# Performance work log

Measured on AMD Instinct MI355X. Metric: run time of the kernel, lower is better.

Reference implementation:

```python
import jax, jax.numpy as jnp
import numpy as np

B, N, PREV, PRED, H = 16, 64, 6, 30, 256
E = N * (N - 1)
BN_EPS = 1e-5


def _mlp(x, W1, b1, W2, b2, gamma, beta):
    # Two-layer ELU MLP with batch norm over flattened (batch*rows) dim.
    h = jax.nn.elu(x @ W1 + b1)
    h = jax.nn.elu(h @ W2 + b2)
    b, n, d = h.shape
    f = h.reshape(b * n, d)
    mu = f.mean(axis=0)
    var = f.var(axis=0)
    f = (f - mu) * jax.lax.rsqrt(var + BN_EPS) * gamma + beta
    return f.reshape(b, n, d)


def setup_inputs() -> dict:
    key = jax.random.key(0)
    ks = jax.random.split(key, 8)
    # fully-connected directed graph without self loops
    recv, send = np.where(~np.eye(N, dtype=bool))  # each [E]
    rel_rec = jnp.broadcast_to(jax.nn.one_hot(jnp.asarray(recv), N)[None], (B, E, N)).astype(jnp.float32)
    rel_send = jnp.broadcast_to(jax.nn.one_hot(jnp.asarray(send), N)[None], (B, E, N)).astype(jnp.float32)

    def xavier(k, shape):
        fan_in, fan_out = shape
        std = np.sqrt(2.0 / (fan_in + fan_out))
        return jax.random.normal(k, shape, jnp.float32) * std

    return {
        "prev_actor_centers": jax.random.normal(ks[0], (B, N, PREV, 2), jnp.float32) * 10.0,
        "rel_rec": rel_rec,
        "rel_send": rel_send,
        "W_traj": xavier(ks[1], (PREV * 2, H)),
        "b_traj": jnp.full((H,), 0.1, jnp.float32),
        "n2e_W1": xavier(ks[2], (2 * H, H)),
        "n2e_b1": jnp.full((H,), 0.1, jnp.float32),
        "n2e_W2": xavier(ks[3], (H, H)),
        "n2e_b2": jnp.full((H,), 0.1, jnp.float32),
        "n2e_gamma": jnp.ones((H,), jnp.float32),
        "n2e_beta": jnp.zeros((H,), jnp.float32),
        "e2n_W1": xavier(ks[4], (2 * H, H)),
        "e2n_b1": jnp.full((H,), 0.1, jnp.float32),
        "e2n_W2": xavier(ks[5], (H, H)),
        "e2n_b2": jnp.full((H,), 0.1, jnp.float32),
        "e2n_gamma": jnp.ones((H,), jnp.float32),
        "e2n_beta": jnp.zeros((H,), jnp.float32),
        "W_fuse": xavier(ks[6], (2 * H, H)),
        "b_fuse": jnp.full((H,), 0.1, jnp.float32),
        "W_pred": xavier(ks[7], (H, PRED * 2)),
        "b_pred": jnp.full((PRED * 2,), 0.1, jnp.float32),
    }


def reference(prev_actor_centers, rel_rec, rel_send,
              W_traj, b_traj,
              n2e_W1, n2e_b1, n2e_W2, n2e_b2, n2e_gamma, n2e_beta,
              e2n_W1, e2n_b1, e2n_W2, e2n_b2, e2n_gamma, e2n_beta,
              W_fuse, b_fuse, W_pred, b_pred):
    b, n, prev, _ = prev_actor_centers.shape
    # relative displacements, first step zero
    diffs = prev_actor_centers[:, :, 1:, :] - prev_actor_centers[:, :, :-1, :]
    rel_pos = jnp.concatenate([jnp.zeros((b, n, 1, 2), prev_actor_centers.dtype), diffs], axis=2)
    rel_pos = rel_pos.reshape(b, n, prev * 2)
    x = rel_pos @ W_traj + b_traj  # [b, n, H] node features

    # node2edge: gather via one-hot relation matmuls
    receivers = jnp.einsum('ben,bnh->beh', rel_rec, x)
    senders = jnp.einsum('ben,bnh->beh', rel_send, x)
    edges = jnp.concatenate([receivers, senders], axis=-1)  # [b, E, 2H]
    e = _mlp(edges, n2e_W1, n2e_b1, n2e_W2, n2e_b2, n2e_gamma, n2e_beta)

    # edge2node: degree-normalized scatter via transposed relation matmuls
    deg_rec = rel_rec.sum(axis=1)  # [b, n]
    deg_rec = deg_rec + (deg_rec == 0).astype(deg_rec.dtype)
    incoming = jnp.einsum('ben,beh->bnh', rel_rec, e) / deg_rec[..., None]
    deg_send = rel_send.sum(axis=1)
    deg_send = deg_send + (deg_send == 0).astype(deg_send.dtype)
    outgoing = jnp.einsum('ben,beh->bnh', rel_send, e) / deg_send[..., None]
    nodes = jnp.concatenate([incoming, outgoing], axis=-1)  # [b, n, 2H]
    m = _mlp(nodes, e2n_W1, e2n_b1, e2n_W2, e2n_b2, e2n_gamma, e2n_beta)

    fused = jnp.concatenate([x, m], axis=-1) @ W_fuse + b_fuse  # [b, n, H]
    rel = fused @ W_pred + b_pred  # [b, n, PRED*2]

    current_loc = prev_actor_centers[:, :, -1, :]  # [b, n, 2]
    current_loc = jnp.broadcast_to(current_loc[:, :, None, :], (b, n, PRED, 2)).reshape(b, n, PRED * 2)
    pos = jnp.cumsum(rel.reshape(b, n, PRED, 2), axis=2).reshape(b, n, PRED * 2) + current_loc
    return (rel, pos)
```

## Files before the change

### kernel.cpp

```cpp
#include <hip/hip_runtime.h>
#include <hip/hip_bf16.h>

#define BB 16
#define NN 64
#define PREVN 6
#define PREDN 30
#define HH 256
#define EE 4032
#define EROWS (BB*EE)
#define NROWS (BB*NN)

typedef short short8 __attribute__((ext_vector_type(8)));
typedef float f32x4 __attribute__((ext_vector_type(4)));

enum : int {
  OFF_STATS_E = 0,
  OFF_STATS_M = 1024,
  OFF_XRS     = 2048,
  F32_END     = 264192
};
enum : size_t {
  BO_W1TE  = 262144,
  BO_W2TE  = 393216,
  BO_W1TN  = 458752,
  BO_W2TN  = 589824,
  BO_WFT   = 655360,
  BO_WPT   = 786432,
  BO_NODES = 802816,
  BO_M2    = 1327104,
  BO_E2    = 1589248
};

__device__ __forceinline__ float eluf(float v) { return v > 0.f ? v : __expf(v) - 1.f; }

__device__ __forceinline__ void gl2lds16(const void* g, void* l) {
  __builtin_amdgcn_global_load_lds(
      (const __attribute__((address_space(1))) void*)g,
      (__attribute__((address_space(3))) void*)l, 16, 0, 0);
}

__device__ __forceinline__ float xembed(const float* __restrict__ centers,
                                        const float* __restrict__ Wt,
                                        const float* __restrict__ bt,
                                        int rr, int col) {
  const float* c = centers + rr * 12;
  float acc = bt[col];
  #pragma unroll
  for (int t = 0; t < 5; ++t) {
    float dx = c[(t+1)*2 + 0] - c[t*2 + 0];
    float dy = c[(t+1)*2 + 1] - c[t*2 + 1];
    acc += dx * Wt[(2 + 2*t)*HH + col] + dy * Wt[(3 + 2*t)*HH + col];
  }
  return acc;
}

struct PrepArgs {
  const float *n2e_W1, *n2e_W2, *e2n_W1, *e2n_W2, *W_fuse, *W_pred;
  float* stats;
  __hip_bfloat16 *w1te, *w2te, *w1tn, *w2tn, *wft, *wpt;
};

__global__ __launch_bounds__(256) void k_prep(PrepArgs a) {
  __shared__ float t[64][65];
  const int bid = blockIdx.x, tid = threadIdx.x;
  if (bid < 128) {
    const float* W; __hip_bfloat16* WT; int K, lb;
    if (bid < 32)      { W = a.n2e_W1; WT = a.w1te; K = 512; lb = bid; }
    else if (bid < 48) { W = a.n2e_W2; WT = a.w2te; K = 256; lb = bid - 32; }
    else if (bid < 80) { W = a.e2n_W1; WT = a.w1tn; K = 512; lb = bid - 48; }
    else if (bid < 96) { W = a.e2n_W2; WT = a.w2tn; K = 256; lb = bid - 80; }
    else               { W = a.W_fuse; WT = a.wft;  K = 512; lb = bid - 96; }
    int KB = K / 64;
    int k0 = (lb % KB) * 64, n0 = (lb / KB) * 64;
    int tx = tid & 63, ty = tid >> 6;
    #pragma unroll
    for (int i = 0; i < 16; ++i)
      t[ty + i*4][tx] = W[(size_t)(k0 + ty + i*4) * 256 + n0 + tx];
    __syncthreads();
    #pragma unroll
    for (int i = 0; i < 16; ++i)
      WT[(size_t)(n0 + ty + i*4) * K + k0 + tx] = __float2bfloat16(t[tx][ty + i*4]);
  } else if (bid < 192) {
    int idx = (bid - 128) * 256 + tid;
    int c = idx >> 8, k = idx & 255;
    a.wpt[idx] = __float2bfloat16(c < 60 ? a.W_pred[k * 60 + c] : 0.f);
  } else {
    a.stats[(bid - 192) * 256 + tid] = 0.f;
  }
}

__global__ __launch_bounds__(256) void k_xrs(
    const float* __restrict__ centers,
    const float* __restrict__ W_traj,
    const float* __restrict__ b_traj,
    const __hip_bfloat16* __restrict__ W1T,
    const float* __restrict__ b1,
    __hip_bfloat16* __restrict__ xrs) {
  __shared__ alignas(16) __hip_bfloat16 xls[32][264];
  const int tid = threadIdx.x;
  const int w = tid >> 6, lane = tid & 63;
  const int m16 = lane & 15, quad = lane >> 4;
  const int ko = quad * 8;
  const int half = blockIdx.x >> 5;
  const int row0 = (blockIdx.x & 31) * 32;
  const int colw = w * 64;
  __hip_bfloat16* dst = xrs + (size_t)half * 262144;

  #pragma unroll 4
  for (int r = 0; r < 32; ++r)
    xls[r][tid] = __float2bfloat16(xembed(centers, W_traj, b_traj, row0 + r, tid));
  __syncthreads();

  f32x4 acc[2][4];
  #pragma unroll
  for (int jt = 0; jt < 4; ++jt) {
    float bv = half ? 0.f : b1[colw + jt*16 + m16];
    #pragma unroll
    for (int mt = 0; mt < 2; ++mt) acc[mt][jt] = (f32x4){bv, bv, bv, bv};
  }
  #pragma unroll
  for (int ks = 0; ks < 8; ++ks) {
    short8 af[2], bf[4];
    #pragma unroll
    for (int mt = 0; mt < 2; ++mt)
      af[mt] = *reinterpret_cast<const short8*>(&xls[mt*16 + m16][ks*32 + ko]);
    #pragma unroll
    for (int jt = 0; jt < 4; ++jt)
      bf[jt] = *reinterpret_cast<const short8*>(
          W1T + (size_t)(colw + jt*16 + m16)*512 + half*256 + ks*32 + ko);
    #pragma unroll
    for (int mt = 0; mt < 2; ++mt)
      #pragma unroll
      for (int jt = 0; jt < 4; ++jt)
        acc[mt][jt] = __builtin_amdgcn_mfma_f32_16x16x32_bf16(af[mt], bf[jt],
                                                              acc[mt][jt], 0, 0, 0);
  }
  #pragma unroll
  for (int mt = 0; mt < 2; ++mt)
    #pragma unroll
    for (int jt = 0; jt < 4; ++jt)
      #pragma unroll
      for (int r = 0; r < 4; ++r)
        dst[(size_t)(row0 + mt*16 + quad*4 + r)*256 + colw + jt*16 + m16] =
            __float2bfloat16(acc[mt][jt][r]);
}

__global__ __launch_bounds__(256, 2) void k_mlp6(
    const __hip_bfloat16* __restrict__ xrs,
    const __hip_bfloat16* __restrict__ W2T,
    const float* __restrict__ b2,
    __hip_bfloat16* __restrict__ outp,
    float* __restrict__ stats) {
  __shared__ alignas(16) char reg1[33792];
  __shared__ alignas(16) __hip_bfloat16 h1s[64][264];
  __shared__ float sst[2][256];
  const int tid = threadIdx.x;
  const int w = tid >> 6, lane = tid & 63;
  const int m16 = lane & 15, quad = lane >> 4;
  const int ko = quad * 8;
  const int blk = blockIdx.x;
  const int bb = blk / 63, lb = blk - bb*63;
  const int row0 = blk * 64;
  const int n0 = (lb * 64) / 63;
  const int colw = w * 64;

  const char* xsb = (const char*)(xrs + 262144 + (size_t)bb*64*256);
  #pragma unroll
  for (int i = 0; i < 8; ++i) {
    int seg = w*8 + i;
    gl2lds16(xsb + seg*1024 + lane*16, reg1 + seg*1024);
  }
  if (w == 0)
    gl2lds16((const char*)(xrs + (size_t)(bb*64 + n0)*256) + lane*16, reg1 + 32768);
  sst[0][tid] = 0.f;
  sst[1][tid] = 0.f;
  __syncthreads();

  {
    const int ty = tid >> 7;
    const int c2 = (tid & 127) * 2;
    #pragma unroll 4
    for (int r2 = 0; r2 < 32; ++r2) {
      int r = ty*32 + r2;
      int e = lb*64 + r;
      int rc = e / 63; int jj = e - rc*63;
      int sd = jj + (jj >= rc ? 1 : 0);
      __hip_bfloat162 xa = *reinterpret_cast<const __hip_bfloat162*>(
          reg1 + 32768 + (rc - n0)*512 + c2*2);
      __hip_bfloat162 xs2 = *reinterpret_cast<const __hip_bfloat162*>(
          reg1 + sd*512 + c2*2);
      __hip_bfloat162 o;
      o.x = __float2bfloat16(eluf(__bfloat162float(xa.x) + __bfloat162float(xs2.x)));
      o.y = __float2bfloat16(eluf(__bfloat162float(xa.y) + __bfloat162float(xs2.y)));
      *reinterpret_cast<__hip_bfloat162*>(&h1s[r][c2]) = o;
    }
  }
  __syncthreads();

  f32x4 acc2[4][4];
  #pragma unroll
  for (int jt = 0; jt < 4; ++jt) {
    float bv = b2[colw + jt*16 + m16];
    #pragma unroll
    for (int mt = 0; mt < 4; ++mt) acc2[mt][jt] = (f32x4){bv, bv, bv, bv};
  }
  #pragma unroll
  for (int kt = 0; kt < 4; ++kt) {
    #pragma unroll
    for (int ks = 0; ks < 2; ++ks) {
      const int k0 = kt*64 + ks*32 + ko;
      short8 af[4], bf[4];
      #pragma unroll
      for (int jt = 0; jt < 4; ++jt)
        bf[jt] = *reinterpret_cast<const short8*>(
            W2T + (size_t)(colw + jt*16 + m16)*256 + k0);
      #pragma unroll
      for (int mt = 0; mt < 4; ++mt)
        af[mt] = *(const short8*)((const char*)h1s +
                     (size_t)(mt*16 + m16)*528 + k0*2);
      #pragma unroll
      for (int mt = 0; mt < 4; ++mt)
        #pragma unroll
        for (int jt = 0; jt < 4; ++jt)
          acc2[mt][jt] = __builtin_amdgcn_mfma_f32_16x16x32_bf16(af[mt], bf[jt],
                                                                 acc2[mt][jt], 0, 0, 0);
    }
  }
  __syncthreads();

  #pragma unroll
  for (int jt = 0; jt < 4; ++jt) {
    float ps = 0.f, pq = 0.f;
    #pragma unroll
    for (int mt = 0; mt < 4; ++mt)
      #pragma unroll
      for (int r = 0; r < 4; ++r) {
        float hv = eluf(acc2[mt][jt][r]);
        h1s[mt*16 + quad*4 + r][colw + jt*16 + m16] = __float2bfloat16(hv);
        ps += hv; pq += hv * hv;
      }
    atomicAdd(&sst[0][colw + jt*16 + m16], ps);
    atomicAdd(&sst[1][colw + jt*16 + m16], pq);
  }
  __syncthreads();

  atomicAdd(&stats[tid], sst[0][tid]);
  atomicAdd(&stats[256 + tid], sst[1][tid]);
  #pragma unroll
  for (int i = 0; i < 8; ++i) {
    int u = i*256 + tid;
    int r = u >> 5, c = (u & 31) * 8;
    *reinterpret_cast<uint4*>(outp + (size_t)(row0 + r)*HH + c) =
        *reinterpret_cast<const uint4*>(&h1s[r][c]);
  }
}

__global__ __launch_bounds__(256, 2) void k_mlp3n(
    const __hip_bfloat16* __restrict__ A,
    const __hip_bfloat16* __restrict__ W1T,
    const float* __restrict__ b1,
    const __hip_bfloat16* __restrict__ W2T,
    const float* __restrict__ b2,
    __hip_bfloat16* __restrict__ outp,
    float* __restrict__ stats) {
  __shared__ alignas(16) __hip_bfloat16 Wt[256 * 64];
  __shared__ alignas(16) __hip_bfloat16 At[16 * 64];
  __shared__ alignas(16) __hip_bfloat16 h1s[16][264];
  const int tid = threadIdx.x;
  const int w = tid >> 6, lane = tid & 63;
  const int m16 = lane & 15, quad = lane >> 4;
  const int ko = quad * 8;
  const int row0 = blockIdx.x * 16;
  const int colw = w * 64;
  const int csub = lane >> 3, jl = lane & 7;
  const int jsrc = jl ^ csub;
  const int swz0 = ((quad)     ^ (m16 & 7)) * 16;
  const int swz1 = ((quad + 4) ^ (m16 & 7)) * 16;

  const __hip_bfloat16 *ar0 = nullptr, *ar1 = nullptr;
  if (w < 2) {
    int r = w * 8 + csub;
    ar0 = A + (size_t)(row0 + r) * 512;
    ar1 = ar0 + 256;
  }

  f32x4 acc[4];
  #pragma unroll
  for (int jt = 0; jt < 4; ++jt) {
    float bv = b1[colw + jt*16 + m16];
    acc[jt] = (f32x4){bv, bv, bv, bv};
  }
  for (int kt = 0; kt < 8; ++kt) {
    const int k0 = kt * 64;
    #pragma unroll
    for (int i = 0; i < 8; ++i) {
      const __hip_bfloat16* gp = W1T + (size_t)(colw + i*8 + csub) * 512 + k0 + jsrc*8;
      gl2lds16(gp, (char*)Wt + w*8192 + i*1024);
    }
    if (w < 2) {
      const __hip_bfloat16* gp = (k0 < 256 ? ar0 + k0 : ar1 + (k0 - 256)) + jsrc*8;
      gl2lds16(gp, (char*)At + w*1024);
    }
    __syncthreads();
    #pragma unroll
    for (int ks = 0; ks < 2; ++ks) {
      const int sw = ks ? swz1 : swz0;
      short8 af = *(const short8*)((const char*)At + m16*128 + sw);
      short8 bf[4];
      #pragma unroll
      for (int jt = 0; jt < 4; ++jt)
        bf[jt] = *(const short8*)((const char*)Wt + (colw + jt*16 + m16)*128 + sw);
      #pragma unroll
      for (int jt = 0; jt < 4; ++jt)
        acc[jt] = __builtin_amdgcn_mfma_f32_16x16x32_bf16(af, bf[jt], acc[jt], 0, 0, 0);
    }
    __syncthreads();
  }
  #pragma unroll
  for (int jt = 0; jt < 4; ++jt)
    #pragma unroll
    for (int r = 0; r < 4; ++r)
      h1s[quad*4 + r][colw + jt*16 + m16] = __float2bfloat16(eluf(acc[jt][r]));
  __syncthreads();

  f32x4 acc2[4];
  #pragma unroll
  for (int jt = 0; jt < 4; ++jt) {
    float bv = b2[colw + jt*16 + m16];
    acc2[jt] = (f32x4){bv, bv, bv, bv};
  }
  #pragma unroll
  for (int kt = 0; kt < 4; ++kt) {
    #pragma unroll
    for (int ks = 0; ks < 2; ++ks) {
      const int k0 = kt*64 + ks*32 + ko;
      short8 af = *(const short8*)((const char*)h1s + (size_t)m16*528 + k0*2);
      short8 bf[4];
      #pragma unroll
      for (int jt = 0; jt < 4; ++jt)
        bf[jt] = *reinterpret_cast<const short8*>(
            W2T + (size_t)(colw + jt*16 + m16)*256 + k0);
      #pragma unroll
      for (int jt = 0; jt < 4; ++jt)
        acc2[jt] = __builtin_amdgcn_mfma_f32_16x16x32_bf16(af, bf[jt], acc2[jt], 0, 0, 0);
    }
  }
  __syncthreads();
  #pragma unroll
  for (int jt = 0; jt < 4; ++jt)
    #pragma unroll
    for (int r = 0; r < 4; ++r)
      h1s[quad*4 + r][colw + jt*16 + m16] = __float2bfloat16(eluf(acc2[jt][r]));
  __syncthreads();

  {
    float s = 0.f, q = 0.f;
    #pragma unroll 8
    for (int r = 0; r < 16; ++r) {
      float v = __bfloat162float(h1s[r][tid]);
      s += v; q += v * v;
    }
    atomicAdd(&stats[tid], s);
    atomicAdd(&stats[256 + tid], q);
  }
  #pragma unroll
  for (int i = 0; i < 2; ++i) {
    int u = i*256 + tid;
    int r = u >> 5, c = (u & 31) * 8;
    *reinterpret_cast<uint4*>(outp + (size_t)(row0 + r)*HH + c) =
        *reinterpret_cast<const uint4*>(&h1s[r][c]);
  }
}

__global__ __launch_bounds__(1024) void k_agg2(const __hip_bfloat16* __restrict__ e2,
                                               const float* __restrict__ st,
                                               const float* __restrict__ gam,
                                               const float* __restrict__ bet,
                                               __hip_bfloat16* __restrict__ nodes) {
  __shared__ float red[32][256];
  const int blk = blockIdx.x;
  const int bn = blk >> 1, half = blk & 1;
  const int b = bn >> 6, n = bn & 63;
  const int tid = threadIdx.x;
  const int c8 = (tid & 31) * 8;
  const int rg = tid >> 5;
  const __hip_bfloat16* base = e2 + (size_t)b * EE * HH;
  float s[8] = {0.f,0.f,0.f,0.f,0.f,0.f,0.f,0.f};
  for (int j = rg; j < 63; j += 32) {
    const __hip_bfloat16* rp;
    if (half == 0) {
      rp = base + (size_t)(n*63 + j)*HH;
    } else {
      int i = j + (j >= n ? 1 : 0);
      int e = i*63 + n - (n > i ? 1 : 0);
      rp = base + (size_t)e*HH;
    }
    union { uint4 u; __hip_bfloat16 h[8]; } v;
    v.u = *reinterpret_cast<const uint4*>(rp + c8);
    #pragma unroll
    for (int jj = 0; jj < 8; ++jj) s[jj] += __bfloat162float(v.h[jj]);
  }
  #pragma unroll
  for (int jj = 0; jj < 8; jj += 4)
    *reinterpret_cast<float4*>(&red[rg][c8 + jj]) =
        (float4){s[jj], s[jj+1], s[jj+2], s[jj+3]};
  __syncthreads();
  if (tid < 256) {
    float S = 0.f;
    #pragma unroll
    for (int r = 0; r < 32; ++r) S += red[r][tid];
    const float inv = 1.f / (float)EROWS;
    float mean = st[tid] * inv;
    float var  = fmaxf(st[256 + tid] * inv - mean*mean, 0.f);
    float a = gam[tid] * rsqrtf(var + 1e-5f);
    float c0 = bet[tid] - mean * a;
    nodes[(size_t)bn*512 + half*256 + tid] = __float2bfloat16(a * S * (1.f/63.f) + c0);
  }
}

__global__ __launch_bounds__(256) void k_head2(
    const float* __restrict__ centers,
    const float* __restrict__ W_traj,
    const float* __restrict__ b_traj,
    const __hip_bfloat16* __restrict__ m2,
    const float* __restrict__ stM,
    const float* __restrict__ gam,
    const float* __restrict__ bet,
    const __hip_bfloat16* __restrict__ WfT,
    const float* __restrict__ bfv,
    const __hip_bfloat16* __restrict__ WpT,
    const float* __restrict__ bp,
    float* __restrict__ out) {
  __shared__ alignas(16) __hip_bfloat16 xs[16][264];
  __shared__ alignas(16) __hip_bfloat16 hs[16][264];
  __shared__ float rl[16][64];
  __shared__ float bnA[256], bnC[256];
  const int tid = threadIdx.x;
  const int w = tid >> 6, lane = tid & 63;
  const int m16 = lane & 15, quad = lane >> 4;
  const int ko = quad * 8;
  const int row0 = blockIdx.x * 16;
  const int colw = w * 64;

  {
    const float inv = 1.f / (float)NROWS;
    float mean = stM[tid] * inv;
    float var  = fmaxf(stM[256 + tid] * inv - mean*mean, 0.f);
    float am = gam[tid] * rsqrtf(var + 1e-5f);
    bnA[tid] = am;
    bnC[tid] = bet[tid] - mean * am;
  }
  #pragma unroll
  for (int r = 0; r < 16; ++r)
    xs[r][tid] = __float2bfloat16(xembed(centers, W_traj, b_traj, row0 + r, tid));
  __syncthreads();

  f32x4 acc[4];
  #pragma unroll
  for (int jt = 0; jt < 4; ++jt) {
    float bv = bfv[colw + jt*16 + m16];
    acc[jt] = (f32x4){bv, bv, bv, bv};
  }
  #pragma unroll
  for (int ks = 0; ks < 16; ++ks) {
    short8 af;
    if (ks < 8) {
      af = *reinterpret_cast<const short8*>(&xs[m16][ks*32 + ko]);
    } else {
      int k0 = (ks - 8)*32 + ko;
      union { uint4 u; __hip_bfloat16 h[8]; } v;
      v.u = *reinterpret_cast<const uint4*>(m2 + (size_t)(row0 + m16)*256 + k0);
      union { short8 s8; __hip_bfloat16 h[8]; } o;
      #pragma unroll
      for (int j = 0; j < 8; ++j)
        o.h[j] = __float2bfloat16(bnA[k0+j] * __bfloat162float(v.h[j]) + bnC[k0+j]);
      af = o.s8;
    }
    short8 bf[4];
    #pragma unroll
    for (int jt = 0; jt < 4; ++jt)
      bf[jt] = *reinterpret_cast<const short8*>(
          WfT + (size_t)(colw + jt*16 + m16)*512 + ks*32 + ko);
    #pragma unroll
    for (int jt = 0; jt < 4; ++jt)
      acc[jt] = __builtin_amdgcn_mfma_f32_16x16x32_bf16(af, bf[jt], acc[jt], 0, 0, 0);
  }
  #pragma unroll
  for (int jt = 0; jt < 4; ++jt)
    #pragma unroll
    for (int r = 0; r < 4; ++r)
      hs[quad*4 + r][colw + jt*16 + m16] = __float2bfloat16(acc[jt][r]);
  __syncthreads();

  if (w == 0) {
    f32x4 acc2[4];
    #pragma unroll
    for (int jt = 0; jt < 4; ++jt) {
      int c = jt*16 + m16;
      float bv = (c < 60) ? bp[c] : 0.f;
      acc2[jt] = (f32x4){bv, bv, bv, bv};
    }
    #pragma unroll
    for (int ks = 0; ks < 8; ++ks) {
      short8 af = *reinterpret_cast<const short8*>(&hs[m16][ks*32 + ko]);
      short8 bf[4];
      #pragma unroll
      for (int jt = 0; jt < 4; ++jt)
        bf[jt] = *reinterpret_cast<const short8*>(
            WpT + (size_t)(jt*16 + m16)*256 + ks*32 + ko);
      #pragma unroll
      for (int jt = 0; jt < 4; ++jt)
        acc2[jt] = __builtin_amdgcn_mfma_f32_16x16x32_bf16(af, bf[jt], acc2[jt], 0, 0, 0);
    }
    #pragma unroll
    for (int jt = 0; jt < 4; ++jt) {
      int c = jt*16 + m16;
      #pragma unroll
      for (int r = 0; r < 4; ++r) {
        int lr = quad*4 + r;
        rl[lr][c] = acc2[jt][r];
        if (c < 60) out[(size_t)(row0 + lr)*60 + c] = acc2[jt][r];
      }
    }
  }
  __syncthreads();

  if (tid < 32) {
    int lr = tid >> 1, xy = tid & 1;
    int grow = row0 + lr;
    float run = centers[(size_t)(grow*PREVN + 5)*2 + xy];
    #pragma unroll
    for (int p = 0; p < PREDN; ++p) {
      run += rl[lr][2*p + xy];
      out[61440 + (size_t)grow*60 + 2*p + xy] = run;
    }
  }
}

extern "C" void kernel_launch(void* const* d_in, const int* in_sizes, int n_in,
                              void* d_out, int out_size, void* d_ws, size_t ws_size,
                              hipStream_t stream) {
  const float* centers = (const float*)d_in[0];
  float* ws = (float*)d_ws;
  __hip_bfloat16* wb = (__hip_bfloat16*)(ws + F32_END);
  __hip_bfloat16* xrs = (__hip_bfloat16*)(ws + OFF_XRS);

  const float* W_traj = (const float*)d_in[3];
  const float* b_traj = (const float*)d_in[4];
  const float* n2e_b1 = (const float*)d_in[6];
  const float* n2e_b2 = (const float*)d_in[8];
  const float* n2e_g  = (const float*)d_in[9];
  const float* n2e_be = (const float*)d_in[10];
  const float* e2n_b1 = (const float*)d_in[12];
  const float* e2n_b2 = (const float*)d_in[14];
  const float* e2n_g  = (const float*)d_in[15];
  const float* e2n_be = (const float*)d_in[16];
  const float* b_fuse = (const float*)d_in[18];
  const float* b_pred = (const float*)d_in[20];

  PrepArgs pa;
  pa.n2e_W1 = (const float*)d_in[5];  pa.n2e_W2 = (const float*)d_in[7];
  pa.e2n_W1 = (const float*)d_in[11]; pa.e2n_W2 = (const float*)d_in[13];
  pa.W_fuse = (const float*)d_in[17]; pa.W_pred = (const float*)d_in[19];
  pa.stats = ws;
  pa.w1te = wb + BO_W1TE; pa.w2te = wb + BO_W2TE;
  pa.w1tn = wb + BO_W1TN; pa.w2tn = wb + BO_W2TN;
  pa.wft = wb + BO_WFT;   pa.wpt = wb + BO_WPT;

  k_prep<<<200, 256, 0, stream>>>(pa);
  k_xrs<<<64, 256, 0, stream>>>(centers, W_traj, b_traj, wb + BO_W1TE, n2e_b1, xrs);
  k_mlp6<<<EROWS/64, 256, 0, stream>>>(xrs, wb + BO_W2TE, n2e_b2,
                                       wb + BO_E2, ws + OFF_STATS_E);
  k_agg2<<<2*NROWS, 1024, 0, stream>>>(wb + BO_E2, ws + OFF_STATS_E, n2e_g, n2e_be,
                                       wb + BO_NODES);
  k_mlp3n<<<NROWS/16, 256, 0, stream>>>(wb + BO_NODES, wb + BO_W1TN, e2n_b1,
                                        wb + BO_W2TN, e2n_b2,
                                        wb + BO_M2, ws + OFF_STATS_M);
  k_head2<<<NROWS/16, 256, 0, stream>>>(centers, W_traj, b_traj, wb + BO_M2,
                                        ws + OFF_STATS_M, e2n_g, e2n_be,
                                        wb + BO_WFT, b_fuse, wb + BO_WPT, b_pred,
                                        (float*)d_out);
}
```

Baseline: 206.3 us.

## Fuse edge-to-node aggregation into edge MLP via atomic accumulation

Instead of writing the full bf16 edge activation tensor and re-reading it in a separate aggregation kernel, the edge MLP kernel now accumulates per-receiver and per-sender sums straight into fp32 buffers with global atomics. The batch-norm affine is applied later, when the node MLP loads its A fragments from those sums, and the agg kernel is removed. This cuts a large global write/read round trip and one launch. In exchange it adds many global float atomics (one per row per column for sender sums), a larger zero-init in prep, and non-deterministic summation order.

```diff
diff --git a/kernel.cpp b/kernel.cpp
--- a/kernel.cpp
+++ b/kernel.cpp
@@ -17,18 +17,18 @@
   OFF_STATS_E = 0,
   OFF_STATS_M = 1024,
   OFF_XRS     = 2048,
-  F32_END     = 264192
+  OFF_SACC    = 264192,
+  OFF_TACC    = 526336,
+  F32_END     = 788480
 };
 enum : size_t {
-  BO_W1TE  = 262144,
-  BO_W2TE  = 393216,
-  BO_W1TN  = 458752,
-  BO_W2TN  = 589824,
-  BO_WFT   = 655360,
-  BO_WPT   = 786432,
-  BO_NODES = 802816,
-  BO_M2    = 1327104,
-  BO_E2    = 1589248
+  BO_W1TE  = 0,
+  BO_W2TE  = 131072,
+  BO_W1TN  = 196608,
+  BO_W2TN  = 327680,
+  BO_WFT   = 393216,
+  BO_WPT   = 524288,
+  BO_M2    = 540672
 };
 
 __device__ __forceinline__ float eluf(float v) { return v > 0.f ? v : __expf(v) - 1.f; }
@@ -56,7 +56,7 @@
 
 struct PrepArgs {
   const float *n2e_W1, *n2e_W2, *e2n_W1, *e2n_W2, *W_fuse, *W_pred;
-  float* stats;
+  float* ws;
   __hip_bfloat16 *w1te, *w2te, *w1tn, *w2tn, *wft, *wpt;
 };
 
@@ -84,8 +84,11 @@
     int idx = (bid - 128) * 256 + tid;
     int c = idx >> 8, k = idx & 255;
     a.wpt[idx] = __float2bfloat16(c < 60 ? a.W_pred[k * 60 + c] : 0.f);
+  } else if (bid < 200) {
+    a.ws[(bid - 192) * 256 + tid] = 0.f;
   } else {
-    a.stats[(bid - 192) * 256 + tid] = 0.f;
+    int idx = (bid - 200) * 1024 + tid * 4;
+    *reinterpret_cast<float4*>(a.ws + OFF_SACC + idx) = (float4){0.f, 0.f, 0.f, 0.f};
   }
 }
 
@@ -149,18 +152,19 @@
     const __hip_bfloat16* __restrict__ xrs,
     const __hip_bfloat16* __restrict__ W2T,
     const float* __restrict__ b2,
-    __hip_bfloat16* __restrict__ outp,
-    float* __restrict__ stats) {
+    float* __restrict__ stats,
+    float* __restrict__ Sacc,
+    float* __restrict__ Tacc) {
   __shared__ alignas(16) char reg1[33792];
   __shared__ alignas(16) __hip_bfloat16 h1s[64][264];
-  __shared__ float sst[2][256];
+  __shared__ int sd64[64];
+  __shared__ int rcf[64];
   const int tid = threadIdx.x;
   const int w = tid >> 6, lane = tid & 63;
   const int m16 = lane & 15, quad = lane >> 4;
   const int ko = quad * 8;
   const int blk = blockIdx.x;
   const int bb = blk / 63, lb = blk - bb*63;
-  const int row0 = blk * 64;
   const int n0 = (lb * 64) / 63;
   const int colw = w * 64;
 
@@ -172,8 +176,12 @@
   }
   if (w == 0)
     gl2lds16((const char*)(xrs + (size_t)(bb*64 + n0)*256) + lane*16, reg1 + 32768);
-  sst[0][tid] = 0.f;
-  sst[1][tid] = 0.f;
+  if (tid < 64) {
+    int e = lb*64 + tid;
+    int rc = e / 63; int jj = e - rc*63;
+    sd64[tid] = jj + (jj >= rc ? 1 : 0);
+    rcf[tid]  = rc - n0;
+  }
   __syncthreads();
 
   {
@@ -182,13 +190,10 @@
     #pragma unroll 4
     for (int r2 = 0; r2 < 32; ++r2) {
       int r = ty*32 + r2;
-      int e = lb*64 + r;
-      int rc = e / 63; int jj = e - rc*63;
-      int sd = jj + (jj >= rc ? 1 : 0);
       __hip_bfloat162 xa = *reinterpret_cast<const __hip_bfloat162*>(
-          reg1 + 32768 + (rc - n0)*512 + c2*2);
+          reg1 + 32768 + rcf[r]*512 + c2*2);
       __hip_bfloat162 xs2 = *reinterpret_cast<const __hip_bfloat162*>(
-          reg1 + sd*512 + c2*2);
+          reg1 + sd64[r]*512 + c2*2);
       __hip_bfloat162 o;
       o.x = __float2bfloat16(eluf(__bfloat162float(xa.x) + __bfloat162float(xs2.x)));
       o.y = __float2bfloat16(eluf(__bfloat162float(xa.y) + __bfloat162float(xs2.y)));
@@ -229,34 +234,39 @@
   __syncthreads();
 
   #pragma unroll
-  for (int jt = 0; jt < 4; ++jt) {
-    float ps = 0.f, pq = 0.f;
-    #pragma unroll
-    for (int mt = 0; mt < 4; ++mt)
-      #pragma unroll
-      for (int r = 0; r < 4; ++r) {
-        float hv = eluf(acc2[mt][jt][r]);
-        h1s[mt*16 + quad*4 + r][colw + jt*16 + m16] = __float2bfloat16(hv);
-        ps += hv; pq += hv * hv;
-      }
-    atomicAdd(&sst[0][colw + jt*16 + m16], ps);
-    atomicAdd(&sst[1][colw + jt*16 + m16], pq);
-  }
-  __syncthreads();
-
-  atomicAdd(&stats[tid], sst[0][tid]);
-  atomicAdd(&stats[256 + tid], sst[1][tid]);
-  #pragma unroll
-  for (int i = 0; i < 8; ++i) {
-    int u = i*256 + tid;
-    int r = u >> 5, c = (u & 31) * 8;
-    *reinterpret_cast<uint4*>(outp + (size_t)(row0 + r)*HH + c) =
-        *reinterpret_cast<const uint4*>(&h1s[r][c]);
+  for (int mt = 0; mt < 4; ++mt)
+    #pragma unroll
+    for (int jt = 0; jt < 4; ++jt)
+      #pragma unroll
+      for (int r = 0; r < 4; ++r)
+        h1s[mt*16 + quad*4 + r][colw + jt*16 + m16] =
+            __float2bfloat16(eluf(acc2[mt][jt][r]));
+  __syncthreads();
+
+  {
+    float s = 0.f, q = 0.f, sr0 = 0.f, sr1 = 0.f;
+    float* TaccB = Tacc + (size_t)bb*64*256;
+    #pragma unroll 8
+    for (int r = 0; r < 64; ++r) {
+      float v = __bfloat162float(h1s[r][tid]);
+      s += v; q += v * v;
+      if (rcf[r] == 0) sr0 += v; else sr1 += v;
+      atomicAdd(&TaccB[sd64[r]*256 + tid], v);
+    }
+    atomicAdd(&stats[tid], s);
+    atomicAdd(&stats[256 + tid], q);
+    float* SaccB = Sacc + (size_t)bb*64*256;
+    atomicAdd(&SaccB[n0*256 + tid], sr0);
+    atomicAdd(&SaccB[(n0+1)*256 + tid], sr1);
   }
 }
 
 __global__ __launch_bounds__(256, 2) void k_mlp3n(
-    const __hip_bfloat16* __restrict__ A,
+    const float* __restrict__ Sacc,
+    const float* __restrict__ Tacc,
+    const float* __restrict__ stE,
+    const float* __restrict__ gamE,
+    const float* __restrict__ betE,
     const __hip_bfloat16* __restrict__ W1T,
     const float* __restrict__ b1,
     const __hip_bfloat16* __restrict__ W2T,
@@ -264,8 +274,8 @@
     __hip_bfloat16* __restrict__ outp,
     float* __restrict__ stats) {
   __shared__ alignas(16) __hip_bfloat16 Wt[256 * 64];
-  __shared__ alignas(16) __hip_bfloat16 At[16 * 64];
   __shared__ alignas(16) __hip_bfloat16 h1s[16][264];
+  __shared__ float bnA[256], bnC[256];
   const int tid = threadIdx.x;
   const int w = tid >> 6, lane = tid & 63;
   const int m16 = lane & 15, quad = lane >> 4;
@@ -277,12 +287,32 @@
   const int swz0 = ((quad)     ^ (m16 & 7)) * 16;
   const int swz1 = ((quad + 4) ^ (m16 & 7)) * 16;
 
-  const __hip_bfloat16 *ar0 = nullptr, *ar1 = nullptr;
-  if (w < 2) {
-    int r = w * 8 + csub;
-    ar0 = A + (size_t)(row0 + r) * 512;
-    ar1 = ar0 + 256;
-  }
+  {
+    const float inv = 1.f / (float)EROWS;
+    float mean = stE[tid] * inv;
+    float var  = fmaxf(stE[256 + tid] * inv - mean*mean, 0.f);
+    float a = gamE[tid] * rsqrtf(var + 1e-5f);
+    bnA[tid] = a * (1.f/63.f);
+    bnC[tid] = betE[tid] - mean * a;
+  }
+
+  auto afrag = [&](int k0) -> short8 {
+    int g = row0 + m16;
+    int kb = k0 & 255;
+    const float* src = (k0 < 256) ? (Sacc + (size_t)g*256 + k0)
+                                  : (Tacc + (size_t)g*256 + kb);
+    float4 v0 = *reinterpret_cast<const float4*>(src);
+    float4 v1 = *reinterpret_cast<const float4*>(src + 4);
+    const float* vp0 = reinterpret_cast<const float*>(&v0);
+    const float* vp1 = reinterpret_cast<const float*>(&v1);
+    union { short8 s8; __hip_bfloat16 h[8]; } o;
+    #pragma unroll
+    for (int j = 0; j < 4; ++j) {
+      o.h[j]     = __float2bfloat16(bnA[kb+j]   * vp0[j] + bnC[kb+j]);
+      o.h[4 + j] = __float2bfloat16(bnA[kb+4+j] * vp1[j] + bnC[kb+4+j]);
+    }
+    return o.s8;
+  };
 
   f32x4 acc[4];
   #pragma unroll
@@ -290,6 +320,7 @@
     float bv = b1[colw + jt*16 + m16];
     acc[jt] = (f32x4){bv, bv, bv, bv};
   }
+  __syncthreads();
   for (int kt = 0; kt < 8; ++kt) {
     const int k0 = kt * 64;
     #pragma unroll
@@ -297,15 +328,11 @@
       const __hip_bfloat16* gp = W1T + (size_t)(colw + i*8 + csub) * 512 + k0 + jsrc*8;
       gl2lds16(gp, (char*)Wt + w*8192 + i*1024);
     }
-    if (w < 2) {
-      const __hip_bfloat16* gp = (k0 < 256 ? ar0 + k0 : ar1 + (k0 - 256)) + jsrc*8;
-      gl2lds16(gp, (char*)At + w*1024);
-    }
     __syncthreads();
     #pragma unroll
     for (int ks = 0; ks < 2; ++ks) {
       const int sw = ks ? swz1 : swz0;
-      short8 af = *(const short8*)((const char*)At + m16*128 + sw);
+      short8 af = afrag(k0 + ks*32 + ko);
       short8 bf[4];
       #pragma unroll
       for (int jt = 0; jt < 4; ++jt)
@@ -369,52 +396,6 @@
     int r = u >> 5, c = (u & 31) * 8;
     *reinterpret_cast<uint4*>(outp + (size_t)(row0 + r)*HH + c) =
         *reinterpret_cast<const uint4*>(&h1s[r][c]);
-  }
-}
-
-__global__ __launch_bounds__(1024) void k_agg2(const __hip_bfloat16* __restrict__ e2,
-                                               const float* __restrict__ st,
-                                               const float* __restrict__ gam,
-                                               const float* __restrict__ bet,
-                                               __hip_bfloat16* __restrict__ nodes) {
-  __shared__ float red[32][256];
-  const int blk = blockIdx.x;
-  const int bn = blk >> 1, half = blk & 1;
-  const int b = bn >> 6, n = bn & 63;
-  const int tid = threadIdx.x;
-  const int c8 = (tid & 31) * 8;
-  const int rg = tid >> 5;
-  const __hip_bfloat16* base = e2 + (size_t)b * EE * HH;
-  float s[8] = {0.f,0.f,0.f,0.f,0.f,0.f,0.f,0.f};
-  for (int j = rg; j < 63; j += 32) {
-    const __hip_bfloat16* rp;
-    if (half == 0) {
-      rp = base + (size_t)(n*63 + j)*HH;
-    } else {
-      int i = j + (j >= n ? 1 : 0);
-      int e = i*63 + n - (n > i ? 1 : 0);
-      rp = base + (size_t)e*HH;
-    }
-    union { uint4 u; __hip_bfloat16 h[8]; } v;
-    v.u = *reinterpret_cast<const uint4*>(rp + c8);
-    #pragma unroll
-    for (int jj = 0; jj < 8; ++jj) s[jj] += __bfloat162float(v.h[jj]);
-  }
-  #pragma unroll
-  for (int jj = 0; jj < 8; jj += 4)
-    *reinterpret_cast<float4*>(&red[rg][c8 + jj]) =
-        (float4){s[jj], s[jj+1], s[jj+2], s[jj+3]};
-  __syncthreads();
-  if (tid < 256) {
-    float S = 0.f;
-    #pragma unroll
-    for (int r = 0; r < 32; ++r) S += red[r][tid];
-    const float inv = 1.f / (float)EROWS;
-    float mean = st[tid] * inv;
-    float var  = fmaxf(st[256 + tid] * inv - mean*mean, 0.f);
-    float a = gam[tid] * rsqrtf(var + 1e-5f);
-    float c0 = bet[tid] - mean * a;
-    nodes[(size_t)bn*512 + half*256 + tid] = __float2bfloat16(a * S * (1.f/63.f) + c0);
   }
 }
 
@@ -562,19 +543,18 @@
   pa.n2e_W1 = (const float*)d_in[5];  pa.n2e_W2 = (const float*)d_in[7];
   pa.e2n_W1 = (const float*)d_in[11]; pa.e2n_W2 = (const float*)d_in[13];
   pa.W_fuse = (const float*)d_in[17]; pa.W_pred = (const float*)d_in[19];
-  pa.stats = ws;
+  pa.ws = ws;
   pa.w1te = wb + BO_W1TE; pa.w2te = wb + BO_W2TE;
   pa.w1tn = wb + BO_W1TN; pa.w2tn = wb + BO_W2TN;
   pa.wft = wb + BO_WFT;   pa.wpt = wb + BO_WPT;
 
-  k_prep<<<200, 256, 0, stream>>>(pa);
+  k_prep<<<712, 256, 0, stream>>>(pa);
   k_xrs<<<64, 256, 0, stream>>>(centers, W_traj, b_traj, wb + BO_W1TE, n2e_b1, xrs);
   k_mlp6<<<EROWS/64, 256, 0, stream>>>(xrs, wb + BO_W2TE, n2e_b2,
-                                       wb + BO_E2, ws + OFF_STATS_E);
-  k_agg2<<<2*NROWS, 1024, 0, stream>>>(wb + BO_E2, ws + OFF_STATS_E, n2e_g, n2e_be,
-                                       wb + BO_NODES);
-  k_mlp3n<<<NROWS/16, 256, 0, stream>>>(wb + BO_NODES, wb + BO_W1TN, e2n_b1,
-                                        wb + BO_W2TN, e2n_b2,
+                                       ws + OFF_STATS_E, ws + OFF_SACC, ws + OFF_TACC);
+  k_mlp3n<<<NROWS/16, 256, 0, stream>>>(ws + OFF_SACC, ws + OFF_TACC,
+                                        ws + OFF_STATS_E, n2e_g, n2e_be,
+                                        wb + BO_W1TN, e2n_b1, wb + BO_W2TN, e2n_b2,
                                         wb + BO_M2, ws + OFF_STATS_M);
   k_head2<<<NROWS/16, 256, 0, stream>>>(centers, W_traj, b_traj, wb + BO_M2,
                                         ws + OFF_STATS_M, e2n_g, e2n_be,
```

Result: slower. 244.0 us (+18.3%).

## Fuse incoming-edge aggregation into edge MLP epilogue via per-node atomic sums

Applied to the files above, without the earlier changes.

The edge MLP kernel now accumulates per-receiver-node column sums of its ELU output in its epilogue. Each 64-row block spans at most two receivers, and the sums are added atomically into a new zeroed fp32 buffer. The aggregation kernel then only gathers the strided sender-side rows, halving its block count and global reads of the edge tensor. The receiver-side sums now come from fp32 values before bf16 rounding. The change also precomputes per-row receiver and sender indices in LDS, and adds extra zeroing work in the prep kernel plus more global atomics.

```diff
diff --git a/kernel.cpp b/kernel.cpp
--- a/kernel.cpp
+++ b/kernel.cpp
@@ -17,18 +17,19 @@
   OFF_STATS_E = 0,
   OFF_STATS_M = 1024,
   OFF_XRS     = 2048,
-  F32_END     = 264192
+  OFF_SACC    = 264192,
+  F32_END     = 526336
 };
 enum : size_t {
-  BO_W1TE  = 262144,
-  BO_W2TE  = 393216,
-  BO_W1TN  = 458752,
-  BO_W2TN  = 589824,
-  BO_WFT   = 655360,
-  BO_WPT   = 786432,
-  BO_NODES = 802816,
-  BO_M2    = 1327104,
-  BO_E2    = 1589248
+  BO_W1TE  = 0,
+  BO_W2TE  = 131072,
+  BO_W1TN  = 196608,
+  BO_W2TN  = 327680,
+  BO_WFT   = 393216,
+  BO_WPT   = 524288,
+  BO_NODES = 540672,
+  BO_M2    = 1064960,
+  BO_E2    = 1327104
 };
 
 __device__ __forceinline__ float eluf(float v) { return v > 0.f ? v : __expf(v) - 1.f; }
@@ -56,7 +57,7 @@
 
 struct PrepArgs {
   const float *n2e_W1, *n2e_W2, *e2n_W1, *e2n_W2, *W_fuse, *W_pred;
-  float* stats;
+  float* ws;
   __hip_bfloat16 *w1te, *w2te, *w1tn, *w2tn, *wft, *wpt;
 };
 
@@ -84,8 +85,11 @@
     int idx = (bid - 128) * 256 + tid;
     int c = idx >> 8, k = idx & 255;
     a.wpt[idx] = __float2bfloat16(c < 60 ? a.W_pred[k * 60 + c] : 0.f);
+  } else if (bid < 200) {
+    a.ws[(bid - 192) * 256 + tid] = 0.f;
   } else {
-    a.stats[(bid - 192) * 256 + tid] = 0.f;
+    int idx = (bid - 200) * 1024 + tid * 4;
+    *reinterpret_cast<float4*>(a.ws + OFF_SACC + idx) = (float4){0.f, 0.f, 0.f, 0.f};
   }
 }
 
@@ -150,10 +154,14 @@
     const __hip_bfloat16* __restrict__ W2T,
     const float* __restrict__ b2,
     __hip_bfloat16* __restrict__ outp,
-    float* __restrict__ stats) {
+    float* __restrict__ stats,
+    float* __restrict__ Sacc) {
   __shared__ alignas(16) char reg1[33792];
   __shared__ alignas(16) __hip_bfloat16 h1s[64][264];
   __shared__ float sst[2][256];
+  __shared__ float ssr[2][256];
+  __shared__ int sd64[64];
+  __shared__ int rcf[64];
   const int tid = threadIdx.x;
   const int w = tid >> 6, lane = tid & 63;
   const int m16 = lane & 15, quad = lane >> 4;
@@ -172,8 +180,14 @@
   }
   if (w == 0)
     gl2lds16((const char*)(xrs + (size_t)(bb*64 + n0)*256) + lane*16, reg1 + 32768);
-  sst[0][tid] = 0.f;
-  sst[1][tid] = 0.f;
+  if (tid < 64) {
+    int e = lb*64 + tid;
+    int rc = e / 63; int jj = e - rc*63;
+    sd64[tid] = jj + (jj >= rc ? 1 : 0);
+    rcf[tid]  = rc - n0;
+  }
+  sst[0][tid] = 0.f; sst[1][tid] = 0.f;
+  ssr[0][tid] = 0.f; ssr[1][tid] = 0.f;
   __syncthreads();
 
   {
@@ -182,13 +196,10 @@
     #pragma unroll 4
     for (int r2 = 0; r2 < 32; ++r2) {
       int r = ty*32 + r2;
-      int e = lb*64 + r;
-      int rc = e / 63; int jj = e - rc*63;
-      int sd = jj + (jj >= rc ? 1 : 0);
       __hip_bfloat162 xa = *reinterpret_cast<const __hip_bfloat162*>(
-          reg1 + 32768 + (rc - n0)*512 + c2*2);
+          reg1 + 32768 + rcf[r]*512 + c2*2);
       __hip_bfloat162 xs2 = *reinterpret_cast<const __hip_bfloat162*>(
-          reg1 + sd*512 + c2*2);
+          reg1 + sd64[r]*512 + c2*2);
       __hip_bfloat162 o;
       o.x = __float2bfloat16(eluf(__bfloat162float(xa.x) + __bfloat162float(xs2.x)));
       o.y = __float2bfloat16(eluf(__bfloat162float(xa.y) + __bfloat162float(xs2.y)));
@@ -230,7 +241,7 @@
 
   #pragma unroll
   for (int jt = 0; jt < 4; ++jt) {
-    float ps = 0.f, pq = 0.f;
+    float ps = 0.f, pq = 0.f, pr0 = 0.f, pr1 = 0.f;
     #pragma unroll
     for (int mt = 0; mt < 4; ++mt)
       #pragma unroll
@@ -238,20 +249,68 @@
         float hv = eluf(acc2[mt][jt][r]);
         h1s[mt*16 + quad*4 + r][colw + jt*16 + m16] = __float2bfloat16(hv);
         ps += hv; pq += hv * hv;
+        if (rcf[mt*16 + quad*4 + r] == 0) pr0 += hv; else pr1 += hv;
       }
-    atomicAdd(&sst[0][colw + jt*16 + m16], ps);
-    atomicAdd(&sst[1][colw + jt*16 + m16], pq);
+    int c = colw + jt*16 + m16;
+    atomicAdd(&sst[0][c], ps);
+    atomicAdd(&sst[1][c], pq);
+    atomicAdd(&ssr[0][c], pr0);
+    atomicAdd(&ssr[1][c], pr1);
   }
   __syncthreads();
 
   atomicAdd(&stats[tid], sst[0][tid]);
   atomicAdd(&stats[256 + tid], sst[1][tid]);
+  atomicAdd(&Sacc[(size_t)(bb*64 + n0)*256 + tid], ssr[0][tid]);
+  atomicAdd(&Sacc[(size_t)(bb*64 + n0 + 1)*256 + tid], ssr[1][tid]);
   #pragma unroll
   for (int i = 0; i < 8; ++i) {
     int u = i*256 + tid;
     int r = u >> 5, c = (u & 31) * 8;
     *reinterpret_cast<uint4*>(outp + (size_t)(row0 + r)*HH + c) =
         *reinterpret_cast<const uint4*>(&h1s[r][c]);
+  }
+}
+
+__global__ __launch_bounds__(1024) void k_agg3(const __hip_bfloat16* __restrict__ e2,
+                                               const float* __restrict__ Sacc,
+                                               const float* __restrict__ st,
+                                               const float* __restrict__ gam,
+                                               const float* __restrict__ bet,
+                                               __hip_bfloat16* __restrict__ nodes) {
+  __shared__ float red[32][256];
+  const int bn = blockIdx.x;
+  const int b = bn >> 6, n = bn & 63;
+  const int tid = threadIdx.x;
+  const int c8 = (tid & 31) * 8;
+  const int rg = tid >> 5;
+  const __hip_bfloat16* base = e2 + (size_t)b * EE * HH;
+  float s[8] = {0.f,0.f,0.f,0.f,0.f,0.f,0.f,0.f};
+  for (int j = rg; j < 63; j += 32) {
+    int i = j + (j >= n ? 1 : 0);
+    int e = i*63 + n - (n > i ? 1 : 0);
+    union { uint4 u; __hip_bfloat16 h[8]; } v;
+    v.u = *reinterpret_cast<const uint4*>(base + (size_t)e*HH + c8);
+    #pragma unroll
+    for (int jj = 0; jj < 8; ++jj) s[jj] += __bfloat162float(v.h[jj]);
+  }
+  #pragma unroll
+  for (int jj = 0; jj < 8; jj += 4)
+    *reinterpret_cast<float4*>(&red[rg][c8 + jj]) =
+        (float4){s[jj], s[jj+1], s[jj+2], s[jj+3]};
+  __syncthreads();
+  if (tid < 256) {
+    float T = 0.f;
+    #pragma unroll
+    for (int r = 0; r < 32; ++r) T += red[r][tid];
+    float S = Sacc[(size_t)bn*256 + tid];
+    const float inv = 1.f / (float)EROWS;
+    float mean = st[tid] * inv;
+    float var  = fmaxf(st[256 + tid] * inv - mean*mean, 0.f);
+    float a = gam[tid] * rsqrtf(var + 1e-5f);
+    float c0 = bet[tid] - mean * a;
+    nodes[(size_t)bn*512 + tid]       = __float2bfloat16(a * S * (1.f/63.f) + c0);
+    nodes[(size_t)bn*512 + 256 + tid] = __float2bfloat16(a * T * (1.f/63.f) + c0);
   }
 }
 
@@ -369,52 +428,6 @@
     int r = u >> 5, c = (u & 31) * 8;
     *reinterpret_cast<uint4*>(outp + (size_t)(row0 + r)*HH + c) =
         *reinterpret_cast<const uint4*>(&h1s[r][c]);
-  }
-}
-
-__global__ __launch_bounds__(1024) void k_agg2(const __hip_bfloat16* __restrict__ e2,
-                                               const float* __restrict__ st,
-                                               const float* __restrict__ gam,
-                                               const float* __restrict__ bet,
-                                               __hip_bfloat16* __restrict__ nodes) {
-  __shared__ float red[32][256];
-  const int blk = blockIdx.x;
-  const int bn = blk >> 1, half = blk & 1;
-  const int b = bn >> 6, n = bn & 63;
-  const int tid = threadIdx.x;
-  const int c8 = (tid & 31) * 8;
-  const int rg = tid >> 5;
-  const __hip_bfloat16* base = e2 + (size_t)b * EE * HH;
-  float s[8] = {0.f,0.f,0.f,0.f,0.f,0.f,0.f,0.f};
-  for (int j = rg; j < 63; j += 32) {
-    const __hip_bfloat16* rp;
-    if (half == 0) {
-      rp = base + (size_t)(n*63 + j)*HH;
-    } else {
-      int i = j + (j >= n ? 1 : 0);
-      int e = i*63 + n - (n > i ? 1 : 0);
-      rp = base + (size_t)e*HH;
-    }
-    union { uint4 u; __hip_bfloat16 h[8]; } v;
-    v.u = *reinterpret_cast<const uint4*>(rp + c8);
-    #pragma unroll
-    for (int jj = 0; jj < 8; ++jj) s[jj] += __bfloat162float(v.h[jj]);
-  }
-  #pragma unroll
-  for (int jj = 0; jj < 8; jj += 4)
-    *reinterpret_cast<float4*>(&red[rg][c8 + jj]) =
-        (float4){s[jj], s[jj+1], s[jj+2], s[jj+3]};
-  __syncthreads();
-  if (tid < 256) {
-    float S = 0.f;
-    #pragma unroll
-    for (int r = 0; r < 32; ++r) S += red[r][tid];
-    const float inv = 1.f / (float)EROWS;
-    float mean = st[tid] * inv;
-    float var  = fmaxf(st[256 + tid] * inv - mean*mean, 0.f);
-    float a = gam[tid] * rsqrtf(var + 1e-5f);
-    float c0 = bet[tid] - mean * a;
-    nodes[(size_t)bn*512 + half*256 + tid] = __float2bfloat16(a * S * (1.f/63.f) + c0);
   }
 }
 
@@ -562,17 +575,17 @@
   pa.n2e_W1 = (const float*)d_in[5];  pa.n2e_W2 = (const float*)d_in[7];
   pa.e2n_W1 = (const float*)d_in[11]; pa.e2n_W2 = (const float*)d_in[13];
   pa.W_fuse = (const float*)d_in[17]; pa.W_pred = (const float*)d_in[19];
-  pa.stats = ws;
+  pa.ws = ws;
   pa.w1te = wb + BO_W1TE; pa.w2te = wb + BO_W2TE;
   pa.w1tn = wb + BO_W1TN; pa.w2tn = wb + BO_W2TN;
   pa.wft = wb + BO_WFT;   pa.wpt = wb + BO_WPT;
 
-  k_prep<<<200, 256, 0, stream>>>(pa);
+  k_prep<<<456, 256, 0, stream>>>(pa);
   k_xrs<<<64, 256, 0, stream>>>(centers, W_traj, b_traj, wb + BO_W1TE, n2e_b1, xrs);
-  k_mlp6<<<EROWS/64, 256, 0, stream>>>(xrs, wb + BO_W2TE, n2e_b2,
-                                       wb + BO_E2, ws + OFF_STATS_E);
-  k_agg2<<<2*NROWS, 1024, 0, stream>>>(wb + BO_E2, ws + OFF_STATS_E, n2e_g, n2e_be,
-                                       wb + BO_NODES);
+  k_mlp6<<<EROWS/64, 256, 0, stream>>>(xrs, wb + BO_W2TE, n2e_b2, wb + BO_E2,
+                                       ws + OFF_STATS_E, ws + OFF_SACC);
+  k_agg3<<<NROWS, 1024, 0, stream>>>(wb + BO_E2, ws + OFF_SACC, ws + OFF_STATS_E,
+                                     n2e_g, n2e_be, wb + BO_NODES);
   k_mlp3n<<<NROWS/16, 256, 0, stream>>>(wb + BO_NODES, wb + BO_W1TN, e2n_b1,
                                         wb + BO_W2TN, e2n_b2,
                                         wb + BO_M2, ws + OFF_STATS_M);
```

New measurement: 215.4 us. 1.04x slower.
